# Kernel optimization log

Hardware: AMD Instinct MI355X
Metric: run time of the kernel (lower is better)

Reference implementation:

```python
import jax, jax.numpy as jnp
import numpy as np

N = 50000
E = 800000
IN_CH = 128
HID = 32
HEADS = 8
OUT_CH = 64
NEG_SLOPE = 0.2  # PyG GATConv default


def setup_inputs() -> dict:
    key = jax.random.key(0)
    ks = jax.random.split(key, 12)
    x = jax.random.normal(ks[0], (N, IN_CH), dtype=jnp.float32)
    edge_index = jax.random.randint(ks[1], (2, E), 0, N, dtype=jnp.int64)
    s = 0.1
    return {
        "x": x,
        "edge_index": edge_index,
        "W1": jax.random.normal(ks[2], (IN_CH, HEADS * HID), dtype=jnp.float32) * s,
        "att_src1": jax.random.normal(ks[3], (HEADS, HID), dtype=jnp.float32) * s,
        "att_dst1": jax.random.normal(ks[4], (HEADS, HID), dtype=jnp.float32) * s,
        "b1": jnp.zeros((HEADS * HID,), dtype=jnp.float32),
        "W2": jax.random.normal(ks[5], (HEADS * HID, OUT_CH), dtype=jnp.float32) * s,
        "att_src2": jax.random.normal(ks[6], (1, OUT_CH), dtype=jnp.float32) * s,
        "att_dst2": jax.random.normal(ks[7], (1, OUT_CH), dtype=jnp.float32) * s,
        "b2": jnp.zeros((OUT_CH,), dtype=jnp.float32),
    }


def _gat_layer(x, src, dst, n, W, a_src, a_dst, b, concat):
    # x: [N, F_in]; src/dst: [E']; W: [F_in, H*C]; a_*: [H, C]
    H, C = a_src.shape
    h = (x @ W).reshape(-1, H, C)                       # [N, H, C]
    alpha_s = jnp.einsum('nhc,hc->nh', h, a_src)        # [N, H]
    alpha_d = jnp.einsum('nhc,hc->nh', h, a_dst)        # [N, H]
    alpha = alpha_s[src] + alpha_d[dst]                 # [E', H]
    alpha = jax.nn.leaky_relu(alpha, NEG_SLOPE)
    # segment (per-destination-node) softmax over incoming edges
    m = jax.ops.segment_max(alpha, dst, num_segments=n)     # [n, H]
    e = jnp.exp(alpha - m[dst])
    denom = jax.ops.segment_sum(e, dst, num_segments=n)     # [n, H]
    coef = e / denom[dst]                                   # [E', H]
    msg = h[src] * coef[:, :, None]                         # [E', H, C]
    out = jax.ops.segment_sum(msg, dst, num_segments=n)     # [n, H, C]
    out = out.reshape(n, H * C) if concat else out.mean(axis=1)
    return out + b


def reference(x, edge_index, W1, att_src1, att_dst1, b1, W2, att_src2, att_dst2, b2):
    n = x.shape[0]
    # PyG GATConv default: add self-loops
    loop = jnp.arange(n, dtype=edge_index.dtype)
    src = jnp.concatenate([edge_index[0], loop])
    dst = jnp.concatenate([edge_index[1], loop])
    # eval mode: F.dropout and attention dropout are identity
    h = _gat_layer(x, src, dst, n, W1, att_src1, att_dst1, b1, concat=True)
    h = jax.nn.elu(h)
    out = _gat_layer(h, src, dst, n, W2, att_src2, att_dst2, b2, concat=False)
    return out
```

## Files before the change

kernel.cpp:

```cpp
#include <hip/hip_runtime.h>
#include <hip/hip_bf16.h>
#include <math.h>

#define N_NODES 50000
#define N_EDGES 800000
#define E_TOT   (N_EDGES + N_NODES)
#define IN_CH 128
#define HID 32
#define HEADS 8
#define OUT_CH 64
#define NEG_SLOPE 0.2f
#define G1BLK 3125
#define G2BLK 782
#define ABLK 12500
#define LOG2E 1.4426950408889634f

#define CHUNK_E 5376
#define NCHUNK 159
#define NBUCK 391
#define CNT_TOT (NBUCK * NCHUNK)
#define SBLK 243

typedef __attribute__((ext_vector_type(8))) short bf16x8;
typedef __attribute__((ext_vector_type(4))) float f32x4;

__device__ __forceinline__ float explrelu(float z) {
    return exp2f(fmaxf(z * LOG2E, z * (NEG_SLOPE * LOG2E)));
}

__device__ __forceinline__ unsigned short f2bf(float f) {
    unsigned int u = __float_as_uint(f);
    unsigned int r = (u + 0x7FFFu + ((u >> 16) & 1u)) >> 16;
    return (unsigned short)r;
}
__device__ __forceinline__ float bf2f(unsigned short u) {
    return __uint_as_float(((unsigned int)u) << 16);
}
__device__ __forceinline__ float bflo(unsigned int u) {
    return __uint_as_float(u << 16);
}
__device__ __forceinline__ float bfhi(unsigned int u) {
    return __uint_as_float(u & 0xFFFF0000u);
}

__global__ __launch_bounds__(256) void hist1_kernel(const int* __restrict__ ei,
                                                    int* __restrict__ cnt) {
    __shared__ int hist[NBUCK];
    int t = threadIdx.x, blk = blockIdx.x;
    for (int j = t; j < NBUCK; j += 256) hist[j] = 0;
    __syncthreads();
#pragma unroll
    for (int i = 0; i < 21; ++i) {
        int e = blk * CHUNK_E + i * 256 + t;
        if (e < E_TOT) {
            int d = (e < N_EDGES) ? ei[N_EDGES + e] : (e - N_EDGES);
            atomicAdd(&hist[d >> 7], 1);
        }
    }
    __syncthreads();
    for (int j = t; j < NBUCK; j += 256) cnt[j * NCHUNK + blk] = hist[j];
}

__global__ void sscan1_kernel(const int* __restrict__ cnt, int* __restrict__ pos,
                              int* __restrict__ bsum) {
    __shared__ int s[256];
    int b = blockIdx.x, t = threadIdx.x, g = b * 256 + t;
    int v = (g < CNT_TOT) ? cnt[g] : 0;
    s[t] = v;
    __syncthreads();
    for (int d = 1; d < 256; d <<= 1) {
        int o = (t >= d) ? s[t - d] : 0;
        __syncthreads();
        s[t] += o;
        __syncthreads();
    }
    if (g < CNT_TOT) pos[g] = s[t] - v;
    if (t == 255) bsum[b] = s[t];
}

__global__ void sscan2_kernel(int* __restrict__ bsum, int nb) {
    __shared__ int s[256];
    int t = threadIdx.x;
    int v = (t < nb) ? bsum[t] : 0;
    s[t] = v;
    __syncthreads();
    for (int d = 1; d < 256; d <<= 1) {
        int o = (t >= d) ? s[t - d] : 0;
        __syncthreads();
        s[t] += o;
        __syncthreads();
    }
    if (t < nb) bsum[t] = s[t] - v;
}

__global__ void sscan3_kernel(int* __restrict__ pos, const int* __restrict__ bsum) {
    int b = blockIdx.x, t = threadIdx.x, g = b * 256 + t;
    if (g < CNT_TOT) pos[g] += bsum[b];
}

__global__ __launch_bounds__(256) void scat1_kernel(const int* __restrict__ ei,
                                                    const int* __restrict__ pos,
                                                    int* __restrict__ tmp_s,
                                                    int* __restrict__ tmp_d) {
    __shared__ int cur[NBUCK];
    int t = threadIdx.x, blk = blockIdx.x;
    for (int j = t; j < NBUCK; j += 256) cur[j] = pos[j * NCHUNK + blk];
    __syncthreads();
#pragma unroll
    for (int i = 0; i < 21; ++i) {
        int e = blk * CHUNK_E + i * 256 + t;
        if (e < E_TOT) {
            int s, d;
            if (e < N_EDGES) { s = ei[e]; d = ei[N_EDGES + e]; }
            else             { s = d = e - N_EDGES; }
            int p = atomicAdd(&cur[d >> 7], 1);
            tmp_s[p] = s;
            tmp_d[p] = d;
        }
    }
}

__global__ __launch_bounds__(256) void l2group_kernel(
    const int* __restrict__ pos, const int* __restrict__ tmp_s,
    const int* __restrict__ tmp_d, int* __restrict__ off, int* __restrict__ ssrc) {
    __shared__ int nc[128];
    __shared__ int sc[128];
    int b = blockIdx.x, t = threadIdx.x;
    int seg_start = pos[b * NCHUNK];
    int seg_end = (b + 1 < NBUCK) ? pos[(b + 1) * NCHUNK] : E_TOT;
    if (t < 128) nc[t] = 0;
    __syncthreads();
    for (int i = seg_start + t; i < seg_end; i += 256)
        atomicAdd(&nc[tmp_d[i] & 127], 1);
    __syncthreads();
    if (t < 128) sc[t] = nc[t];
    __syncthreads();
    for (int dd = 1; dd < 128; dd <<= 1) {
        int v = 0;
        if (t < 128 && t >= dd) v = sc[t - dd];
        __syncthreads();
        if (t < 128) sc[t] += v;
        __syncthreads();
    }
    if (t < 128) {
        int excl = sc[t] - nc[t];
        int node = b * 128 + t;
        if (node < N_NODES) off[node] = seg_start + excl;
        nc[t] = seg_start + excl;
    }
    if (b == 0 && t == 0) off[N_NODES] = E_TOT;
    __syncthreads();
    for (int i = seg_start + t; i < seg_end; i += 256) {
        int d = tmp_d[i];
        int p = atomicAdd(&nc[d & 127], 1);
        ssrc[p] = tmp_s[i];
    }
}

__global__ void w1cast_kernel(const float* __restrict__ W1,
                              unsigned short* __restrict__ W1t) {
    int i = blockIdx.x * 256 + threadIdx.x;
    int col = i >> 7, k = i & 127;
    W1t[i] = f2bf(W1[k * 256 + col]);
}

__global__ void w2cast_kernel(const float* __restrict__ W2,
                              unsigned short* __restrict__ W2t) {
    int i = blockIdx.x * 256 + threadIdx.x;
    int col = i >> 8, k = i & 255;
    W2t[i] = f2bf(W2[k * 64 + col]);
}

__global__ __launch_bounds__(256) void gemm1_mfma(
    const float* __restrict__ x, const unsigned short* __restrict__ W1t,
    const float* __restrict__ att_s, const float* __restrict__ att_d,
    unsigned short* __restrict__ h1b, float* __restrict__ as1, float* __restrict__ ad1) {
    int t = threadIdx.x;
    int lane = t & 63;
    int w = t >> 6;
    int lrow = lane & 15;
    int kg = lane >> 4;
    int row0 = blockIdx.x * 16;
    int gr = row0 + lrow;
    f32x4 acc0 = {0.f, 0.f, 0.f, 0.f};
    f32x4 acc1 = {0.f, 0.f, 0.f, 0.f};
    f32x4 acc2 = {0.f, 0.f, 0.f, 0.f};
    f32x4 acc3 = {0.f, 0.f, 0.f, 0.f};
#pragma unroll
    for (int ks = 0; ks < 4; ++ks) {
        const float* ap = &x[(size_t)gr * IN_CH + ks * 32 + kg * 8];
        float4 a0 = *(const float4*)ap;
        float4 a1 = *(const float4*)(ap + 4);
        union { bf16x8 v; unsigned int u[4]; } A;
        A.u[0] = ((unsigned)f2bf(a0.y) << 16) | f2bf(a0.x);
        A.u[1] = ((unsigned)f2bf(a0.w) << 16) | f2bf(a0.z);
        A.u[2] = ((unsigned)f2bf(a1.y) << 16) | f2bf(a1.x);
        A.u[3] = ((unsigned)f2bf(a1.w) << 16) | f2bf(a1.z);
        union { bf16x8 v; uint4 u; } B0, B1, B2, B3;
        int kb = ks * 32 + kg * 8;
        B0.u = *(const uint4*)&W1t[(size_t)(w * 64 + 0 * 16 + lrow) * IN_CH + kb];
        B1.u = *(const uint4*)&W1t[(size_t)(w * 64 + 1 * 16 + lrow) * IN_CH + kb];
        B2.u = *(const uint4*)&W1t[(size_t)(w * 64 + 2 * 16 + lrow) * IN_CH + kb];
        B3.u = *(const uint4*)&W1t[(size_t)(w * 64 + 3 * 16 + lrow) * IN_CH + kb];
        acc0 = __builtin_amdgcn_mfma_f32_16x16x32_bf16(A.v, B0.v, acc0, 0, 0, 0);
        acc1 = __builtin_amdgcn_mfma_f32_16x16x32_bf16(A.v, B1.v, acc1, 0, 0, 0);
        acc2 = __builtin_amdgcn_mfma_f32_16x16x32_bf16(A.v, B2.v, acc2, 0, 0, 0);
        acc3 = __builtin_amdgcn_mfma_f32_16x16x32_bf16(A.v, B3.v, acc3, 0, 0, 0);
    }
    float s0 = att_s[w * 64 + 0 * 16 + lrow], d0 = att_d[w * 64 + 0 * 16 + lrow];
    float s1 = att_s[w * 64 + 1 * 16 + lrow], d1 = att_d[w * 64 + 1 * 16 + lrow];
    float s2 = att_s[w * 64 + 2 * 16 + lrow], d2 = att_d[w * 64 + 2 * 16 + lrow];
    float s3 = att_s[w * 64 + 3 * 16 + lrow], d3 = att_d[w * 64 + 3 * 16 + lrow];
#pragma unroll
    for (int r = 0; r < 4; ++r) {
        int orow = row0 + kg * 4 + r;
        h1b[(size_t)orow * 256 + w * 64 +  0 + lrow] = f2bf(acc0[r]);
        h1b[(size_t)orow * 256 + w * 64 + 16 + lrow] = f2bf(acc1[r]);
        h1b[(size_t)orow * 256 + w * 64 + 32 + lrow] = f2bf(acc2[r]);
        h1b[(size_t)orow * 256 + w * 64 + 48 + lrow] = f2bf(acc3[r]);
        float p0 = acc0[r] * s0 + acc1[r] * s1;
        float q0 = acc0[r] * d0 + acc1[r] * d1;
        float p1 = acc2[r] * s2 + acc3[r] * s3;
        float q1 = acc2[r] * d2 + acc3[r] * d3;
        p0 += __shfl_xor(p0, 1); q0 += __shfl_xor(q0, 1);
        p1 += __shfl_xor(p1, 1); q1 += __shfl_xor(q1, 1);
        p0 += __shfl_xor(p0, 2); q0 += __shfl_xor(q0, 2);
        p1 += __shfl_xor(p1, 2); q1 += __shfl_xor(q1, 2);
        p0 += __shfl_xor(p0, 4); q0 += __shfl_xor(q0, 4);
        p1 += __shfl_xor(p1, 4); q1 += __shfl_xor(q1, 4);
        p0 += __shfl_xor(p0, 8); q0 += __shfl_xor(q0, 8);
        p1 += __shfl_xor(p1, 8); q1 += __shfl_xor(q1, 8);
        if (lrow == 0) {
            as1[orow * HEADS + 2 * w]     = p0;
            ad1[orow * HEADS + 2 * w]     = q0;
            as1[orow * HEADS + 2 * w + 1] = p1;
            ad1[orow * HEADS + 2 * w + 1] = q1;
        }
    }
}

__global__ __launch_bounds__(256) void agg1_kernel(
    const int* __restrict__ off, const int* __restrict__ ssrc,
    const unsigned short* __restrict__ h1b, const float* __restrict__ as1,
    const float* __restrict__ ad1, const float* __restrict__ b1,
    unsigned short* __restrict__ houtb) {
    int t = threadIdx.x;
    int lane = t & 63;
    int n = blockIdx.x * 4 + (t >> 6);
    int h    = lane >> 3;
    int e8   = lane & 7;
    int c    = lane & 31;
    int hh   = c >> 2;
    int half = lane >> 5;
    int start = off[n], end = off[n + 1];
    int last = end - 1;
    float ad_w = ad1[n * HEADS + e8];
    float acc[8];
#pragma unroll
    for (int j = 0; j < 8; ++j) acc[j] = 0.f;
    float den = 0.f;
    int sv = ssrc[min(start + e8, last)];
    int se = __shfl(sv, h);
    float av = as1[se * HEADS + e8];
    const unsigned short* base = h1b + c * 8;
    uint4 g0 = *(const uint4*)&base[(unsigned)__shfl(sv, 0 + half) * 256];
    uint4 g1 = *(const uint4*)&base[(unsigned)__shfl(sv, 2 + half) * 256];
    uint4 g2 = *(const uint4*)&base[(unsigned)__shfl(sv, 4 + half) * 256];
    uint4 g3 = *(const uint4*)&base[(unsigned)__shfl(sv, 6 + half) * 256];
    for (int i = start; i < end; i += 8) {
        int inext = i + 8;
        int sv_n = ssrc[min(inext + e8, last)];
        int se_n = __shfl(sv_n, h);
        float av_n = as1[se_n * HEADS + e8];
        uint4 n0 = *(const uint4*)&base[(unsigned)__shfl(sv_n, 0 + half) * 256];
        uint4 n1 = *(const uint4*)&base[(unsigned)__shfl(sv_n, 2 + half) * 256];
        uint4 n2 = *(const uint4*)&base[(unsigned)__shfl(sv_n, 4 + half) * 256];
        uint4 n3 = *(const uint4*)&base[(unsigned)__shfl(sv_n, 6 + half) * 256];
        float wv = explrelu(av + ad_w);
        float w0 = __shfl(wv, (0 + half) * 8 + hh);
        float w1 = __shfl(wv, (2 + half) * 8 + hh);
        float w2 = __shfl(wv, (4 + half) * 8 + hh);
        float w3 = __shfl(wv, (6 + half) * 8 + hh);
        w0 = (i + 0 + half < end) ? w0 : 0.f;
        w1 = (i + 2 + half < end) ? w1 : 0.f;
        w2 = (i + 4 + half < end) ? w2 : 0.f;
        w3 = (i + 6 + half < end) ? w3 : 0.f;
        den += w0 + w1 + w2 + w3;
        acc[0] = fmaf(w0, bflo(g0.x), acc[0]); acc[1] = fmaf(w0, bfhi(g0.x), acc[1]);
        acc[2] = fmaf(w0, bflo(g0.y), acc[2]); acc[3] = fmaf(w0, bfhi(g0.y), acc[3]);
        acc[4] = fmaf(w0, bflo(g0.z), acc[4]); acc[5] = fmaf(w0, bfhi(g0.z), acc[5]);
        acc[6] = fmaf(w0, bflo(g0.w), acc[6]); acc[7] = fmaf(w0, bfhi(g0.w), acc[7]);
        acc[0] = fmaf(w1, bflo(g1.x), acc[0]); acc[1] = fmaf(w1, bfhi(g1.x), acc[1]);
        acc[2] = fmaf(w1, bflo(g1.y), acc[2]); acc[3] = fmaf(w1, bfhi(g1.y), acc[3]);
        acc[4] = fmaf(w1, bflo(g1.z), acc[4]); acc[5] = fmaf(w1, bfhi(g1.z), acc[5]);
        acc[6] = fmaf(w1, bflo(g1.w), acc[6]); acc[7] = fmaf(w1, bfhi(g1.w), acc[7]);
        acc[0] = fmaf(w2, bflo(g2.x), acc[0]); acc[1] = fmaf(w2, bfhi(g2.x), acc[1]);
        acc[2] = fmaf(w2, bflo(g2.y), acc[2]); acc[3] = fmaf(w2, bfhi(g2.y), acc[3]);
        acc[4] = fmaf(w2, bflo(g2.z), acc[4]); acc[5] = fmaf(w2, bfhi(g2.z), acc[5]);
        acc[6] = fmaf(w2, bflo(g2.w), acc[6]); acc[7] = fmaf(w2, bfhi(g2.w), acc[7]);
        acc[0] = fmaf(w3, bflo(g3.x), acc[0]); acc[1] = fmaf(w3, bfhi(g3.x), acc[1]);
        acc[2] = fmaf(w3, bflo(g3.y), acc[2]); acc[3] = fmaf(w3, bfhi(g3.y), acc[3]);
        acc[4] = fmaf(w3, bflo(g3.z), acc[4]); acc[5] = fmaf(w3, bfhi(g3.z), acc[5]);
        acc[6] = fmaf(w3, bflo(g3.w), acc[6]); acc[7] = fmaf(w3, bfhi(g3.w), acc[7]);
        g0 = n0; g1 = n1; g2 = n2; g3 = n3;
        sv = sv_n; av = av_n;
    }
#pragma unroll
    for (int j = 0; j < 8; ++j) acc[j] += __shfl_xor(acc[j], 32);
    den += __shfl_xor(den, 32);
    if (lane < 32) {
        float r = __builtin_amdgcn_rcpf(den);
        float4 b0 = *(const float4*)&b1[c * 8];
        float4 b4 = *(const float4*)&b1[c * 8 + 4];
        float v0 = fmaf(acc[0], r, b0.x);
        float v1 = fmaf(acc[1], r, b0.y);
        float v2 = fmaf(acc[2], r, b0.z);
        float v3 = fmaf(acc[3], r, b0.w);
        float v4 = fmaf(acc[4], r, b4.x);
        float v5 = fmaf(acc[5], r, b4.y);
        float v6 = fmaf(acc[6], r, b4.z);
        float v7 = fmaf(acc[7], r, b4.w);
        v0 = v0 > 0.f ? v0 : expm1f(v0);
        v1 = v1 > 0.f ? v1 : expm1f(v1);
        v2 = v2 > 0.f ? v2 : expm1f(v2);
        v3 = v3 > 0.f ? v3 : expm1f(v3);
        v4 = v4 > 0.f ? v4 : expm1f(v4);
        v5 = v5 > 0.f ? v5 : expm1f(v5);
        v6 = v6 > 0.f ? v6 : expm1f(v6);
        v7 = v7 > 0.f ? v7 : expm1f(v7);
        uint4 ob;
        ob.x = (unsigned)f2bf(v0) | ((unsigned)f2bf(v1) << 16);
        ob.y = (unsigned)f2bf(v2) | ((unsigned)f2bf(v3) << 16);
        ob.z = (unsigned)f2bf(v4) | ((unsigned)f2bf(v5) << 16);
        ob.w = (unsigned)f2bf(v6) | ((unsigned)f2bf(v7) << 16);
        *(uint4*)&houtb[(unsigned)n * 256 + c * 8] = ob;
    }
}

__global__ __launch_bounds__(256) void gemm2_mfma(
    const unsigned short* __restrict__ hinb, const unsigned short* __restrict__ W2t,
    const float* __restrict__ att_s2, const float* __restrict__ att_d2,
    unsigned short* __restrict__ h2b, float* __restrict__ as2, float* __restrict__ ad2) {
    int t = threadIdx.x;
    int lane = t & 63;
    int w = t >> 6;
    int lrow = lane & 15;
    int kg = lane >> 4;
    int row0 = blockIdx.x * 64 + w * 16;
    int gr = min(row0 + lrow, N_NODES - 1);
    f32x4 acc0 = {0.f, 0.f, 0.f, 0.f};
    f32x4 acc1 = {0.f, 0.f, 0.f, 0.f};
    f32x4 acc2 = {0.f, 0.f, 0.f, 0.f};
    f32x4 acc3 = {0.f, 0.f, 0.f, 0.f};
#pragma unroll
    for (int ks = 0; ks < 8; ++ks) {
        int kb = ks * 32 + kg * 8;
        union { bf16x8 v; uint4 u; } A, B0, B1, B2, B3;
        A.u  = *(const uint4*)&hinb[(size_t)gr * 256 + kb];
        B0.u = *(const uint4*)&W2t[(size_t)(0 * 16 + lrow) * 256 + kb];
        B1.u = *(const uint4*)&W2t[(size_t)(1 * 16 + lrow) * 256 + kb];
        B2.u = *(const uint4*)&W2t[(size_t)(2 * 16 + lrow) * 256 + kb];
        B3.u = *(const uint4*)&W2t[(size_t)(3 * 16 + lrow) * 256 + kb];
        acc0 = __builtin_amdgcn_mfma_f32_16x16x32_bf16(A.v, B0.v, acc0, 0, 0, 0);
        acc1 = __builtin_amdgcn_mfma_f32_16x16x32_bf16(A.v, B1.v, acc1, 0, 0, 0);
        acc2 = __builtin_amdgcn_mfma_f32_16x16x32_bf16(A.v, B2.v, acc2, 0, 0, 0);
        acc3 = __builtin_amdgcn_mfma_f32_16x16x32_bf16(A.v, B3.v, acc3, 0, 0, 0);
    }
    float s0 = att_s2[ 0 + lrow], d0 = att_d2[ 0 + lrow];
    float s1 = att_s2[16 + lrow], d1 = att_d2[16 + lrow];
    float s2 = att_s2[32 + lrow], d2 = att_d2[32 + lrow];
    float s3 = att_s2[48 + lrow], d3 = att_d2[48 + lrow];
#pragma unroll
    for (int r = 0; r < 4; ++r) {
        int orow = row0 + kg * 4 + r;
        float p = acc0[r] * s0 + acc1[r] * s1 + acc2[r] * s2 + acc3[r] * s3;
        float q = acc0[r] * d0 + acc1[r] * d1 + acc2[r] * d2 + acc3[r] * d3;
        p += __shfl_xor(p, 1); q += __shfl_xor(q, 1);
        p += __shfl_xor(p, 2); q += __shfl_xor(q, 2);
        p += __shfl_xor(p, 4); q += __shfl_xor(q, 4);
        p += __shfl_xor(p, 8); q += __shfl_xor(q, 8);
        if (orow < N_NODES) {
            h2b[(size_t)orow * 64 +  0 + lrow] = f2bf(acc0[r]);
            h2b[(size_t)orow * 64 + 16 + lrow] = f2bf(acc1[r]);
            h2b[(size_t)orow * 64 + 32 + lrow] = f2bf(acc2[r]);
            h2b[(size_t)orow * 64 + 48 + lrow] = f2bf(acc3[r]);
            if (lrow == 0) { as2[orow] = p; ad2[orow] = q; }
        }
    }
}

__global__ __launch_bounds__(256) void agg2_kernel(
    const int* __restrict__ off, const int* __restrict__ ssrc,
    const unsigned short* __restrict__ h2b, const float* __restrict__ as2,
    const float* __restrict__ ad2, const float* __restrict__ b2,
    float* __restrict__ out) {
    int t = threadIdx.x;
    int lane = t & 63;
    int e8 = lane & 7;
    int q = lane & 15;
    int quarter = lane >> 4;
    int n = blockIdx.x * 4 + (t >> 6);
    int start = off[n], end = off[n + 1];
    int last = end - 1;
    float adv = ad2[n];
    float acc[4];
#pragma unroll
    for (int j = 0; j < 4; ++j) acc[j] = 0.f;
    float den = 0.f;
    int sv = ssrc[min(start + e8, last)];
    float av = as2[sv];
    for (int i = start; i < end; i += 8) {
        int inext = i + 8;
        int sv_n = ssrc[min(inext + e8, last)];
        float av_n = as2[sv_n];
        float wv = explrelu(av + adv);
#pragma unroll
        for (int k = 0; k < 2; ++k) {
            int me = 4 * k + quarter;
            float wj = __shfl(wv, me);
            int   sj = __shfl(sv, me);
            wj = (i + me < end) ? wj : 0.f;
            uint2 u = *(const uint2*)&h2b[(unsigned)sj * 64 + q * 4];
            den += wj;
            acc[0] = fmaf(wj, bflo(u.x), acc[0]);
            acc[1] = fmaf(wj, bfhi(u.x), acc[1]);
            acc[2] = fmaf(wj, bflo(u.y), acc[2]);
            acc[3] = fmaf(wj, bfhi(u.y), acc[3]);
        }
        sv = sv_n; av = av_n;
    }
#pragma unroll
    for (int j = 0; j < 4; ++j) {
        acc[j] += __shfl_xor(acc[j], 16);
        acc[j] += __shfl_xor(acc[j], 32);
    }
    den += __shfl_xor(den, 16);
    den += __shfl_xor(den, 32);
    if (lane < 16) {
        float r = __builtin_amdgcn_rcpf(den);
        float4 bv = *(const float4*)&b2[q * 4];
        float4 o;
        o.x = fmaf(acc[0], r, bv.x);
        o.y = fmaf(acc[1], r, bv.y);
        o.z = fmaf(acc[2], r, bv.z);
        o.w = fmaf(acc[3], r, bv.w);
        *(float4*)&out[(unsigned)n * 64 + q * 4] = o;
    }
}

extern "C" void kernel_launch(void* const* d_in, const int* in_sizes, int n_in,
                              void* d_out, int out_size, void* d_ws, size_t ws_size,
                              hipStream_t stream) {
    const float* x    = (const float*)d_in[0];
    const int*   ei   = (const int*)d_in[1];
    const float* W1   = (const float*)d_in[2];
    const float* ats1 = (const float*)d_in[3];
    const float* atd1 = (const float*)d_in[4];
    const float* b1   = (const float*)d_in[5];
    const float* W2   = (const float*)d_in[6];
    const float* ats2 = (const float*)d_in[7];
    const float* atd2 = (const float*)d_in[8];
    const float* b2   = (const float*)d_in[9];
    float* out = (float*)d_out;

    char* ws = (char*)d_ws;
    size_t o = 0;
    auto alloc = [&](size_t bytes) { size_t r = o; o = (o + bytes + 255) & ~255UL; return r; };
    unsigned short* h1b   = (unsigned short*)(ws + alloc((size_t)N_NODES * 256 * 2));
    unsigned short* h2inb = (unsigned short*)(ws + alloc((size_t)N_NODES * 256 * 2));
    unsigned short* h2b   = (unsigned short*)(ws + alloc((size_t)N_NODES * 64 * 2));
    unsigned short* W1t   = (unsigned short*)(ws + alloc((size_t)256 * 128 * 2));
    unsigned short* W2t   = (unsigned short*)(ws + alloc((size_t)64 * 256 * 2));
    float* as1  = (float*)(ws + alloc((size_t)N_NODES * HEADS * 4));
    float* ad1  = (float*)(ws + alloc((size_t)N_NODES * HEADS * 4));
    float* as2  = (float*)(ws + alloc((size_t)N_NODES * 4));
    float* ad2  = (float*)(ws + alloc((size_t)N_NODES * 4));
    int*   cnt  = (int*)(ws + alloc((size_t)CNT_TOT * 4));
    int*   pos  = (int*)(ws + alloc((size_t)CNT_TOT * 4));
    int*   bsum = (int*)(ws + alloc(256 * 4));
    int*   off  = (int*)(ws + alloc((size_t)(N_NODES + 1) * 4));
    int*   tmp_s = (int*)(ws + alloc((size_t)E_TOT * 4));
    int*   tmp_d = (int*)(ws + alloc((size_t)E_TOT * 4));
    int*   ssrc  = (int*)(ws + alloc((size_t)E_TOT * 4));

    hist1_kernel<<<NCHUNK, 256, 0, stream>>>(ei, cnt);
    sscan1_kernel<<<SBLK, 256, 0, stream>>>(cnt, pos, bsum);
    sscan2_kernel<<<1, 256, 0, stream>>>(bsum, SBLK);
    sscan3_kernel<<<SBLK, 256, 0, stream>>>(pos, bsum);
    scat1_kernel<<<NCHUNK, 256, 0, stream>>>(ei, pos, tmp_s, tmp_d);
    l2group_kernel<<<NBUCK, 256, 0, stream>>>(pos, tmp_s, tmp_d, off, ssrc);

    w1cast_kernel<<<128, 256, 0, stream>>>(W1, W1t);
    gemm1_mfma<<<G1BLK, 256, 0, stream>>>(x, W1t, ats1, atd1, h1b, as1, ad1);
    agg1_kernel<<<ABLK, 256, 0, stream>>>(off, ssrc, h1b, as1, ad1, b1, h2inb);

    w2cast_kernel<<<64, 256, 0, stream>>>(W2, W2t);
    gemm2_mfma<<<G2BLK, 256, 0, stream>>>(h2inb, W2t, ats2, atd2, h2b, as2, ad2);
    agg2_kernel<<<ABLK, 256, 0, stream>>>(off, ssrc, h2b, as2, ad2, b2, out);
}
```

Before: 206.1 us.

## Merge independent preprocessing and GEMM launches into shared-grid fused kernels

Independent kernels now share one launch, with blocks split by block index: the edge histogram runs alongside the W1 cast, the edge scatter alongside the layer-1 GEMM, and the per-node grouping alongside the W2 cast. This takes the launch count from 12 to 9, removing launch gaps and letting small, latency-bound graph-preprocessing kernels overlap with compute work. The cost is that each fused kernel has a larger static shared-memory footprint and register pressure that apply to every block, which could lower GEMM occupancy.

```diff
diff --git a/kernel.cpp b/kernel.cpp
--- a/kernel.cpp
+++ b/kernel.cpp
@@ -43,22 +43,29 @@
     return __uint_as_float(u & 0xFFFF0000u);
 }
 
-__global__ __launch_bounds__(256) void hist1_kernel(const int* __restrict__ ei,
-                                                    int* __restrict__ cnt) {
+__global__ __launch_bounds__(256) void fuseA_kernel(
+    const int* __restrict__ ei, int* __restrict__ cnt,
+    const float* __restrict__ W1, unsigned short* __restrict__ W1t) {
     __shared__ int hist[NBUCK];
-    int t = threadIdx.x, blk = blockIdx.x;
-    for (int j = t; j < NBUCK; j += 256) hist[j] = 0;
-    __syncthreads();
-#pragma unroll
-    for (int i = 0; i < 21; ++i) {
-        int e = blk * CHUNK_E + i * 256 + t;
-        if (e < E_TOT) {
-            int d = (e < N_EDGES) ? ei[N_EDGES + e] : (e - N_EDGES);
-            atomicAdd(&hist[d >> 7], 1);
-        }
-    }
-    __syncthreads();
-    for (int j = t; j < NBUCK; j += 256) cnt[j * NCHUNK + blk] = hist[j];
+    int t = threadIdx.x, b = blockIdx.x;
+    if (b < NCHUNK) {
+        for (int j = t; j < NBUCK; j += 256) hist[j] = 0;
+        __syncthreads();
+#pragma unroll
+        for (int i = 0; i < 21; ++i) {
+            int e = b * CHUNK_E + i * 256 + t;
+            if (e < E_TOT) {
+                int d = (e < N_EDGES) ? ei[N_EDGES + e] : (e - N_EDGES);
+                atomicAdd(&hist[d >> 7], 1);
+            }
+        }
+        __syncthreads();
+        for (int j = t; j < NBUCK; j += 256) cnt[j * NCHUNK + b] = hist[j];
+    } else {
+        int i = (b - NCHUNK) * 256 + t;
+        int col = i >> 7, k = i & 127;
+        W1t[i] = f2bf(W1[k * 256 + col]);
+    }
 }
 
 __global__ void sscan1_kernel(const int* __restrict__ cnt, int* __restrict__ pos,
@@ -98,89 +105,16 @@
     if (g < CNT_TOT) pos[g] += bsum[b];
 }
 
-__global__ __launch_bounds__(256) void scat1_kernel(const int* __restrict__ ei,
-                                                    const int* __restrict__ pos,
-                                                    int* __restrict__ tmp_s,
-                                                    int* __restrict__ tmp_d) {
-    __shared__ int cur[NBUCK];
-    int t = threadIdx.x, blk = blockIdx.x;
-    for (int j = t; j < NBUCK; j += 256) cur[j] = pos[j * NCHUNK + blk];
-    __syncthreads();
-#pragma unroll
-    for (int i = 0; i < 21; ++i) {
-        int e = blk * CHUNK_E + i * 256 + t;
-        if (e < E_TOT) {
-            int s, d;
-            if (e < N_EDGES) { s = ei[e]; d = ei[N_EDGES + e]; }
-            else             { s = d = e - N_EDGES; }
-            int p = atomicAdd(&cur[d >> 7], 1);
-            tmp_s[p] = s;
-            tmp_d[p] = d;
-        }
-    }
-}
-
-__global__ __launch_bounds__(256) void l2group_kernel(
-    const int* __restrict__ pos, const int* __restrict__ tmp_s,
-    const int* __restrict__ tmp_d, int* __restrict__ off, int* __restrict__ ssrc) {
-    __shared__ int nc[128];
-    __shared__ int sc[128];
-    int b = blockIdx.x, t = threadIdx.x;
-    int seg_start = pos[b * NCHUNK];
-    int seg_end = (b + 1 < NBUCK) ? pos[(b + 1) * NCHUNK] : E_TOT;
-    if (t < 128) nc[t] = 0;
-    __syncthreads();
-    for (int i = seg_start + t; i < seg_end; i += 256)
-        atomicAdd(&nc[tmp_d[i] & 127], 1);
-    __syncthreads();
-    if (t < 128) sc[t] = nc[t];
-    __syncthreads();
-    for (int dd = 1; dd < 128; dd <<= 1) {
-        int v = 0;
-        if (t < 128 && t >= dd) v = sc[t - dd];
-        __syncthreads();
-        if (t < 128) sc[t] += v;
-        __syncthreads();
-    }
-    if (t < 128) {
-        int excl = sc[t] - nc[t];
-        int node = b * 128 + t;
-        if (node < N_NODES) off[node] = seg_start + excl;
-        nc[t] = seg_start + excl;
-    }
-    if (b == 0 && t == 0) off[N_NODES] = E_TOT;
-    __syncthreads();
-    for (int i = seg_start + t; i < seg_end; i += 256) {
-        int d = tmp_d[i];
-        int p = atomicAdd(&nc[d & 127], 1);
-        ssrc[p] = tmp_s[i];
-    }
-}
-
-__global__ void w1cast_kernel(const float* __restrict__ W1,
-                              unsigned short* __restrict__ W1t) {
-    int i = blockIdx.x * 256 + threadIdx.x;
-    int col = i >> 7, k = i & 127;
-    W1t[i] = f2bf(W1[k * 256 + col]);
-}
-
-__global__ void w2cast_kernel(const float* __restrict__ W2,
-                              unsigned short* __restrict__ W2t) {
-    int i = blockIdx.x * 256 + threadIdx.x;
-    int col = i >> 8, k = i & 255;
-    W2t[i] = f2bf(W2[k * 64 + col]);
-}
-
-__global__ __launch_bounds__(256) void gemm1_mfma(
+__device__ __forceinline__ void gemm1_body(
+    int blk, int t,
     const float* __restrict__ x, const unsigned short* __restrict__ W1t,
     const float* __restrict__ att_s, const float* __restrict__ att_d,
     unsigned short* __restrict__ h1b, float* __restrict__ as1, float* __restrict__ ad1) {
-    int t = threadIdx.x;
     int lane = t & 63;
     int w = t >> 6;
     int lrow = lane & 15;
     int kg = lane >> 4;
-    int row0 = blockIdx.x * 16;
+    int row0 = blk * 16;
     int gr = row0 + lrow;
     f32x4 acc0 = {0.f, 0.f, 0.f, 0.f};
     f32x4 acc1 = {0.f, 0.f, 0.f, 0.f};
@@ -236,6 +170,78 @@
             as1[orow * HEADS + 2 * w + 1] = p1;
             ad1[orow * HEADS + 2 * w + 1] = q1;
         }
+    }
+}
+
+__global__ __launch_bounds__(256) void fuseB_kernel(
+    const int* __restrict__ ei, const int* __restrict__ pos,
+    int* __restrict__ tmp_s, int* __restrict__ tmp_d,
+    const float* __restrict__ x, const unsigned short* __restrict__ W1t,
+    const float* __restrict__ att_s, const float* __restrict__ att_d,
+    unsigned short* __restrict__ h1b, float* __restrict__ as1, float* __restrict__ ad1) {
+    int t = threadIdx.x, b = blockIdx.x;
+    if (b < NCHUNK) {
+        __shared__ int cur[NBUCK];
+        for (int j = t; j < NBUCK; j += 256) cur[j] = pos[j * NCHUNK + b];
+        __syncthreads();
+#pragma unroll
+        for (int i = 0; i < 21; ++i) {
+            int e = b * CHUNK_E + i * 256 + t;
+            if (e < E_TOT) {
+                int s, d;
+                if (e < N_EDGES) { s = ei[e]; d = ei[N_EDGES + e]; }
+                else             { s = d = e - N_EDGES; }
+                int p = atomicAdd(&cur[d >> 7], 1);
+                tmp_s[p] = s;
+                tmp_d[p] = d;
+            }
+        }
+    } else {
+        gemm1_body(b - NCHUNK, t, x, W1t, att_s, att_d, h1b, as1, ad1);
+    }
+}
+
+__global__ __launch_bounds__(256) void fuseC_kernel(
+    const int* __restrict__ pos, const int* __restrict__ tmp_s,
+    const int* __restrict__ tmp_d, int* __restrict__ off, int* __restrict__ ssrc,
+    const float* __restrict__ W2, unsigned short* __restrict__ W2t) {
+    int b = blockIdx.x, t = threadIdx.x;
+    if (b < NBUCK) {
+        __shared__ int nc[128];
+        __shared__ int sc[128];
+        int seg_start = pos[b * NCHUNK];
+        int seg_end = (b + 1 < NBUCK) ? pos[(b + 1) * NCHUNK] : E_TOT;
+        if (t < 128) nc[t] = 0;
+        __syncthreads();
+        for (int i = seg_start + t; i < seg_end; i += 256)
+            atomicAdd(&nc[tmp_d[i] & 127], 1);
+        __syncthreads();
+        if (t < 128) sc[t] = nc[t];
+        __syncthreads();
+        for (int dd = 1; dd < 128; dd <<= 1) {
+            int v = 0;
+            if (t < 128 && t >= dd) v = sc[t - dd];
+            __syncthreads();
+            if (t < 128) sc[t] += v;
+            __syncthreads();
+        }
+        if (t < 128) {
+            int excl = sc[t] - nc[t];
+            int node = b * 128 + t;
+            if (node < N_NODES) off[node] = seg_start + excl;
+            nc[t] = seg_start + excl;
+        }
+        if (b == 0 && t == 0) off[N_NODES] = E_TOT;
+        __syncthreads();
+        for (int i = seg_start + t; i < seg_end; i += 256) {
+            int d = tmp_d[i];
+            int p = atomicAdd(&nc[d & 127], 1);
+            ssrc[p] = tmp_s[i];
+        }
+    } else {
+        int i = (b - NBUCK) * 256 + t;
+        int col = i >> 8, k = i & 255;
+        W2t[i] = f2bf(W2[k * 64 + col]);
     }
 }
 
@@ -483,18 +489,16 @@
     int*   tmp_d = (int*)(ws + alloc((size_t)E_TOT * 4));
     int*   ssrc  = (int*)(ws + alloc((size_t)E_TOT * 4));
 
-    hist1_kernel<<<NCHUNK, 256, 0, stream>>>(ei, cnt);
+    fuseA_kernel<<<NCHUNK + 128, 256, 0, stream>>>(ei, cnt, W1, W1t);
     sscan1_kernel<<<SBLK, 256, 0, stream>>>(cnt, pos, bsum);
     sscan2_kernel<<<1, 256, 0, stream>>>(bsum, SBLK);
     sscan3_kernel<<<SBLK, 256, 0, stream>>>(pos, bsum);
-    scat1_kernel<<<NCHUNK, 256, 0, stream>>>(ei, pos, tmp_s, tmp_d);
-    l2group_kernel<<<NBUCK, 256, 0, stream>>>(pos, tmp_s, tmp_d, off, ssrc);
-
-    w1cast_kernel<<<128, 256, 0, stream>>>(W1, W1t);
-    gemm1_mfma<<<G1BLK, 256, 0, stream>>>(x, W1t, ats1, atd1, h1b, as1, ad1);
+    fuseB_kernel<<<NCHUNK + G1BLK, 256, 0, stream>>>(
+        ei, pos, tmp_s, tmp_d, x, W1t, ats1, atd1, h1b, as1, ad1);
+    fuseC_kernel<<<NBUCK + 64, 256, 0, stream>>>(pos, tmp_s, tmp_d, off, ssrc, W2, W2t);
+
     agg1_kernel<<<ABLK, 256, 0, stream>>>(off, ssrc, h1b, as1, ad1, b1, h2inb);
 
-    w2cast_kernel<<<64, 256, 0, stream>>>(W2, W2t);
     gemm2_mfma<<<G2BLK, 256, 0, stream>>>(h2inb, W2t, ats2, atd2, h2b, as2, ad2);
     agg2_kernel<<<ABLK, 256, 0, stream>>>(off, ssrc, h2b, as2, ad2, b2, out);
 }
```

After: 192.0 us. 6.8% less time.
